# Kernel optimization log

Hardware: AMD Instinct MI355X
Metric: run time of the kernel (lower is better)

The kernel has to match this reference:

```python
import jax, jax.numpy as jnp
import numpy as np

N = 100000
IN_DIM = 128
HID = 128
HEADS = 2
OUT_DIM = 2
E = 800000
NEG_SLOPE = 0.2


def setup_inputs() -> dict:
    key = jax.random.key(0)
    ks = jax.random.split(key, 12)
    x = jax.random.normal(ks[0], (N, IN_DIM), dtype=jnp.float32)
    edge_index = jax.random.randint(ks[1], (2, E), 0, N, dtype=jnp.int64)
    s = 0.05
    # GATConv layer 1: in=128 -> heads=2, out=128
    W1 = jax.random.normal(ks[2], (IN_DIM, HEADS * HID), dtype=jnp.float32) * s
    a_src1 = jax.random.normal(ks[3], (HEADS, HID), dtype=jnp.float32) * s
    a_dst1 = jax.random.normal(ks[4], (HEADS, HID), dtype=jnp.float32) * s
    b1 = jnp.zeros((HEADS * HID,), dtype=jnp.float32)
    # GATConv layer 2: in=256 -> heads=2, out=128
    W2 = jax.random.normal(ks[5], (HEADS * HID, HEADS * HID), dtype=jnp.float32) * s
    a_src2 = jax.random.normal(ks[6], (HEADS, HID), dtype=jnp.float32) * s
    a_dst2 = jax.random.normal(ks[7], (HEADS, HID), dtype=jnp.float32) * s
    b2 = jnp.zeros((HEADS * HID,), dtype=jnp.float32)
    # post_mp: Linear(256,128) -> Dropout(eval, no-op) -> Linear(128,2)
    Wp1 = jax.random.normal(ks[8], (HEADS * HID, HID), dtype=jnp.float32) * s
    bp1 = jnp.zeros((HID,), dtype=jnp.float32)
    Wp2 = jax.random.normal(ks[9], (HID, OUT_DIM), dtype=jnp.float32) * s
    bp2 = jnp.zeros((OUT_DIM,), dtype=jnp.float32)
    return {"x": x, "edge_index": edge_index,
            "W1": W1, "a_src1": a_src1, "a_dst1": a_dst1, "b1": b1,
            "W2": W2, "a_src2": a_src2, "a_dst2": a_dst2, "b2": b2,
            "Wp1": Wp1, "bp1": bp1, "Wp2": Wp2, "bp2": bp2}


def gat_conv(x, src, dst, W, a_src, a_dst, b):
    # linear transform, split heads: [N, H, C]
    h = (x @ W).reshape(-1, HEADS, HID)
    # per-node attention logits: [N, H]
    alpha_src = jnp.sum(h * a_src, axis=-1)
    alpha_dst = jnp.sum(h * a_dst, axis=-1)
    # per-edge logits, edge e = (src -> dst): [E, H]
    e = jax.nn.leaky_relu(alpha_src[src] + alpha_dst[dst], NEG_SLOPE)
    # segment softmax over incoming edges of each destination node
    m = jax.ops.segment_max(e, dst, num_segments=N)
    e = jnp.exp(e - m[dst])
    denom = jax.ops.segment_sum(e, dst, num_segments=N)
    alpha = e / (denom[dst] + 1e-16)
    # gather source features, weight, scatter-add to destinations
    msg = h[src] * alpha[:, :, None]            # [E, H, C]
    out = jax.ops.segment_sum(msg, dst, num_segments=N)  # [N, H, C]
    return out.reshape(-1, HEADS * HID) + b


def reference(x, edge_index, W1, a_src1, a_dst1, b1, W2, a_src2, a_dst2, b2,
              Wp1, bp1, Wp2, bp2):
    # add self-loops (PyG GATConv default)
    loops = jnp.arange(N, dtype=edge_index.dtype)
    src = jnp.concatenate([edge_index[0], loops])
    dst = jnp.concatenate([edge_index[1], loops])
    h = jax.nn.relu(gat_conv(x, src, dst, W1, a_src1, a_dst1, b1))
    h = jax.nn.relu(gat_conv(h, src, dst, W2, a_src2, a_dst2, b2))
    h = h @ Wp1 + bp1          # post_mp Linear 1 (dropout is eval no-op)
    h = h @ Wp2 + bp2          # post_mp Linear 2
    return jax.nn.sigmoid(h)
```

## Files before the change

### kernel.cpp

```cpp
#include <hip/hip_runtime.h>
#include <hip/hip_bf16.h>
#include <math.h>

#define NNODES 100000
#define NPAD   100032
#define IN_DIM 128
#define HID 128
#define HEADS 2
#define F2 256
#define NEDGES 800000
#define ETOT 900000
#define NEG_SLOPE 0.2f

typedef unsigned int uint;
typedef unsigned short ushort;
typedef __attribute__((ext_vector_type(8))) short short8;
typedef __attribute__((ext_vector_type(4))) float floatx4;

__device__ __forceinline__ ushort f2bf(float f) {
    uint u = __builtin_bit_cast(uint, f);
    u += 0x7fffu + ((u >> 16) & 1u);
    return (ushort)(u >> 16);
}
__device__ __forceinline__ float bf2f(uint u16) {
    return __builtin_bit_cast(float, u16 << 16);
}
__device__ __forceinline__ float wred_sum(float v) {
    for (int o = 32; o; o >>= 1) v += __shfl_xor(v, o);
    return v;
}

__global__ __launch_bounds__(256) void hist_kernel(const int* __restrict__ ei,
                                                   int* __restrict__ deg) {
    int i = blockIdx.x * 256 + threadIdx.x;
    if (i >= ETOT) return;
    int dst = (i < NEDGES) ? ei[NEDGES + i] : (i - NEDGES);
    atomicAdd(&deg[dst], 1);
}

__global__ __launch_bounds__(256) void scan1_kernel(const int* __restrict__ deg,
                                                    int* __restrict__ row_start,
                                                    int* __restrict__ bsum) {
    __shared__ int s[256];
    int t = threadIdx.x;
    int i = blockIdx.x * 256 + t;
    int v = (i < NNODES) ? deg[i] : 0;
    s[t] = v;
    __syncthreads();
    for (int off = 1; off < 256; off <<= 1) {
        int x = (t >= off) ? s[t - off] : 0;
        __syncthreads();
        s[t] += x;
        __syncthreads();
    }
    if (i < NNODES) row_start[i] = s[t] - v;
    if (t == 255) bsum[blockIdx.x] = s[255];
}

__global__ __launch_bounds__(512) void scan2_kernel(const int* __restrict__ bsum,
                                                    int* __restrict__ bsum2,
                                                    int cnt) {
    __shared__ int s[512];
    int t = threadIdx.x;
    int v = (t < cnt) ? bsum[t] : 0;
    s[t] = v;
    __syncthreads();
    for (int off = 1; off < 512; off <<= 1) {
        int x = (t >= off) ? s[t - off] : 0;
        __syncthreads();
        s[t] += x;
        __syncthreads();
    }
    bsum2[t] = s[t] - v;
}

__global__ __launch_bounds__(256) void scan3_kernel(int* __restrict__ row_start,
                                                    const int* __restrict__ bsum2,
                                                    int* __restrict__ cursor) {
    int i = blockIdx.x * 256 + threadIdx.x;
    if (i == 0) row_start[NNODES] = ETOT;
    if (i >= NNODES) return;
    int r = row_start[i] + bsum2[i >> 8];
    row_start[i] = r;
    cursor[i] = r;
}

__global__ __launch_bounds__(256) void scatter_kernel(const int* __restrict__ ei,
                                                      int* __restrict__ cursor,
                                                      int* __restrict__ csr_src) {
    int i = blockIdx.x * 256 + threadIdx.x;
    if (i >= ETOT) return;
    int src, dst;
    if (i < NEDGES) { src = ei[i]; dst = ei[NEDGES + i]; }
    else            { src = i - NEDGES; dst = src; }
    int pos = atomicAdd(&cursor[dst], 1);
    csr_src[pos] = src;
}

__global__ __launch_bounds__(256) void transpose_bf_kernel(const float* __restrict__ W,
                                                           ushort* __restrict__ Wt,
                                                           int K, int N) {
    int i = blockIdx.x * 256 + threadIdx.x;
    if (i >= K * N) return;
    int n = i / K, k = i - n * K;
    Wt[(size_t)n * K + k] = f2bf(W[(size_t)k * N + n]);
}

__global__ __launch_bounds__(256) void fw_kernel(const float* __restrict__ Wp1,
                                                 const float* __restrict__ bp1,
                                                 const float* __restrict__ Wp2,
                                                 const float* __restrict__ bp2,
                                                 float2* __restrict__ Wf,
                                                 float* __restrict__ bfv) {
    int k = threadIdx.x;
    float s0 = 0.f, s1 = 0.f;
    for (int m = 0; m < 128; m++) {
        float w = Wp1[(size_t)k * 128 + m];
        s0 += w * Wp2[2 * m];
        s1 += w * Wp2[2 * m + 1];
    }
    Wf[k] = make_float2(s0, s1);
    if (k < 2) {
        float b = bp2[k];
        for (int m = 0; m < 128; m++) b += bp1[m] * Wp2[2 * m + k];
        bfv[k] = b;
    }
}

__global__ __launch_bounds__(256) void mfma_gemm_f32A(const float* __restrict__ A,
                                                      const ushort* __restrict__ Bt,
                                                      ushort* __restrict__ C,
                                                      float* __restrict__ as_f,
                                                      float* __restrict__ ad_f,
                                                      const float* __restrict__ aS,
                                                      const float* __restrict__ aD,
                                                      int K) {
    __shared__ ushort As[64][40];
    __shared__ ushort Bs[128][40];
    int t = threadIdx.x;
    int wave = t >> 6, lane = t & 63;
    int quad = lane >> 4, l16 = lane & 15;
    size_t rowBase = (size_t)blockIdx.x * 64;
    int colBase = blockIdx.y * 128;
    int head = blockIdx.y;

    floatx4 acc[8];
#pragma unroll
    for (int i = 0; i < 8; i++) acc[i] = (floatx4){0.f, 0.f, 0.f, 0.f};

    int ar = t >> 2, ac = (t & 3) * 8;
    int agr = (int)rowBase + ar;
    const float*  Ap  = A + (size_t)agr * K + ac;
    const ushort* Bp0 = Bt + (size_t)(colBase + ar) * K + ac;
    const ushort* Bp1 = Bp0 + (size_t)64 * K;
    bool aok = agr < NNODES;

    for (int k0 = 0; k0 < K; k0 += 32) {
        float4 f0 = make_float4(0.f, 0.f, 0.f, 0.f), f1 = f0;
        if (aok) {
            f0 = *reinterpret_cast<const float4*>(Ap + k0);
            f1 = *reinterpret_cast<const float4*>(Ap + k0 + 4);
        }
        uint4 b0 = *reinterpret_cast<const uint4*>(Bp0 + k0);
        uint4 b1 = *reinterpret_cast<const uint4*>(Bp1 + k0);
        uint4 av;
        av.x = (uint)f2bf(f0.x) | ((uint)f2bf(f0.y) << 16);
        av.y = (uint)f2bf(f0.z) | ((uint)f2bf(f0.w) << 16);
        av.z = (uint)f2bf(f1.x) | ((uint)f2bf(f1.y) << 16);
        av.w = (uint)f2bf(f1.z) | ((uint)f2bf(f1.w) << 16);
        *reinterpret_cast<uint4*>(&As[ar][ac])      = av;
        *reinterpret_cast<uint4*>(&Bs[ar][ac])      = b0;
        *reinterpret_cast<uint4*>(&Bs[64 + ar][ac]) = b1;
        __syncthreads();

        union { uint4 u; short8 s; } afr, bfr;
        afr.u = *reinterpret_cast<const uint4*>(&As[wave * 16 + l16][quad * 8]);
#pragma unroll
        for (int nt = 0; nt < 8; nt++) {
            bfr.u = *reinterpret_cast<const uint4*>(&Bs[nt * 16 + l16][quad * 8]);
            acc[nt] = __builtin_amdgcn_mfma_f32_16x16x32_bf16(afr.s, bfr.s, acc[nt], 0, 0, 0);
        }
        __syncthreads();
    }

#pragma unroll
    for (int nt = 0; nt < 8; nt++) {
        int col = colBase + nt * 16 + l16;
#pragma unroll
        for (int r = 0; r < 4; r++) {
            size_t row = rowBase + wave * 16 + quad * 4 + r;
            C[row * F2 + col] = f2bf(acc[nt][r]);
        }
    }
    float aSv[8], aDv[8];
#pragma unroll
    for (int nt = 0; nt < 8; nt++) {
        int c = colBase + nt * 16 + l16;
        aSv[nt] = aS[c];
        aDv[nt] = aD[c];
    }
#pragma unroll
    for (int r = 0; r < 4; r++) {
        float ps = 0.f, pd = 0.f;
#pragma unroll
        for (int nt = 0; nt < 8; nt++) {
            ps += acc[nt][r] * aSv[nt];
            pd += acc[nt][r] * aDv[nt];
        }
#pragma unroll
        for (int o = 1; o < 16; o <<= 1) {
            ps += __shfl_xor(ps, o);
            pd += __shfl_xor(pd, o);
        }
        if (l16 == 0) {
            size_t row = rowBase + wave * 16 + quad * 4 + r;
            as_f[2 * row + head] = ps;
            ad_f[2 * row + head] = pd;
        }
    }
}

__global__ __launch_bounds__(256) void mfma_gemm_bf16A(const ushort* __restrict__ A,
                                                       const ushort* __restrict__ Bt,
                                                       ushort* __restrict__ C,
                                                       float* __restrict__ as_f,
                                                       float* __restrict__ ad_f,
                                                       const float* __restrict__ aS,
                                                       const float* __restrict__ aD,
                                                       int K) {
    __shared__ ushort As[64][40];
    __shared__ ushort Bs[128][40];
    int t = threadIdx.x;
    int wave = t >> 6, lane = t & 63;
    int quad = lane >> 4, l16 = lane & 15;
    size_t rowBase = (size_t)blockIdx.x * 64;
    int colBase = blockIdx.y * 128;
    int head = blockIdx.y;

    floatx4 acc[8];
#pragma unroll
    for (int i = 0; i < 8; i++) acc[i] = (floatx4){0.f, 0.f, 0.f, 0.f};

    int ar = t >> 2, ac = (t & 3) * 8;
    const ushort* Ap  = A + (rowBase + ar) * K + ac;
    const ushort* Bp0 = Bt + (size_t)(colBase + ar) * K + ac;
    const ushort* Bp1 = Bp0 + (size_t)64 * K;

    for (int k0 = 0; k0 < K; k0 += 32) {
        uint4 av = *reinterpret_cast<const uint4*>(Ap + k0);
        uint4 b0 = *reinterpret_cast<const uint4*>(Bp0 + k0);
        uint4 b1 = *reinterpret_cast<const uint4*>(Bp1 + k0);
        *reinterpret_cast<uint4*>(&As[ar][ac])      = av;
        *reinterpret_cast<uint4*>(&Bs[ar][ac])      = b0;
        *reinterpret_cast<uint4*>(&Bs[64 + ar][ac]) = b1;
        __syncthreads();

        union { uint4 u; short8 s; } afr, bfr;
        afr.u = *reinterpret_cast<const uint4*>(&As[wave * 16 + l16][quad * 8]);
#pragma unroll
        for (int nt = 0; nt < 8; nt++) {
            bfr.u = *reinterpret_cast<const uint4*>(&Bs[nt * 16 + l16][quad * 8]);
            acc[nt] = __builtin_amdgcn_mfma_f32_16x16x32_bf16(afr.s, bfr.s, acc[nt], 0, 0, 0);
        }
        __syncthreads();
    }

#pragma unroll
    for (int nt = 0; nt < 8; nt++) {
        int col = colBase + nt * 16 + l16;
#pragma unroll
        for (int r = 0; r < 4; r++) {
            size_t row = rowBase + wave * 16 + quad * 4 + r;
            C[row * F2 + col] = f2bf(acc[nt][r]);
        }
    }
    float aSv[8], aDv[8];
#pragma unroll
    for (int nt = 0; nt < 8; nt++) {
        int c = colBase + nt * 16 + l16;
        aSv[nt] = aS[c];
        aDv[nt] = aD[c];
    }
#pragma unroll
    for (int r = 0; r < 4; r++) {
        float ps = 0.f, pd = 0.f;
#pragma unroll
        for (int nt = 0; nt < 8; nt++) {
            ps += acc[nt][r] * aSv[nt];
            pd += acc[nt][r] * aDv[nt];
        }
#pragma unroll
        for (int o = 1; o < 16; o <<= 1) {
            ps += __shfl_xor(ps, o);
            pd += __shfl_xor(pd, o);
        }
        if (l16 == 0) {
            size_t row = rowBase + wave * 16 + quad * 4 + r;
            as_f[2 * row + head] = ps;
            ad_f[2 * row + head] = pd;
        }
    }
}

__global__ __launch_bounds__(256) void gather_kernel(const uint2* __restrict__ hb2,
                                                     const int* __restrict__ row_start,
                                                     const int* __restrict__ csr_src,
                                                     const float2* __restrict__ as_,
                                                     const float2* __restrict__ ad_,
                                                     const float4* __restrict__ bias4,
                                                     uint2* __restrict__ outb2,
                                                     const float4* __restrict__ WfA,
                                                     const float* __restrict__ bfv,
                                                     float2* __restrict__ outp,
                                                     int final_mode) {
    int wave = threadIdx.x >> 6, lane = threadIdx.x & 63;
    int n = blockIdx.x * 4 + wave;
    if (n >= NNODES) return;
    int beg = row_start[n], end = row_start[n + 1];
    float2 ad = ad_[n];
    bool head1 = lane >= 32;

    float a0 = 0.f, a1 = 0.f, a2 = 0.f, a3 = 0.f;
    float aden = 0.f;

    for (int chunk = beg; chunk < end; chunk += 64) {
        int cnt = end - chunk;
        if (cnt > 64) cnt = 64;
        int e = chunk + lane;
        int sv = csr_src[(e < end) ? e : (end - 1)];
        float2 q = as_[sv];
        float l0 = q.x + ad.x; l0 = l0 > 0.f ? l0 : NEG_SLOPE * l0;
        float l1 = q.y + ad.y; l1 = l1 > 0.f ? l1 : NEG_SLOPE * l1;
        float w0 = __expf(l0);
        float w1 = __expf(l1);

#pragma unroll 4
        for (int j = 0; j < cnt; j++) {
            int   sj  = __builtin_amdgcn_readlane(sv, j);
            float wj0 = __builtin_bit_cast(float,
                          __builtin_amdgcn_readlane(__builtin_bit_cast(int, w0), j));
            float wj1 = __builtin_bit_cast(float,
                          __builtin_amdgcn_readlane(__builtin_bit_cast(int, w1), j));
            float wj = head1 ? wj1 : wj0;
            uint2 hv = hb2[(size_t)sj * 64 + lane];
            aden += wj;
            a0 += wj * bf2f(hv.x & 0xffffu);
            a1 += wj * bf2f(hv.x >> 16);
            a2 += wj * bf2f(hv.y & 0xffffu);
            a3 += wj * bf2f(hv.y >> 16);
        }
    }
    float inv = 1.f / (aden + 1e-16f);
    float4 b = bias4[lane];
    float o0 = fmaxf(a0 * inv + b.x, 0.f);
    float o1 = fmaxf(a1 * inv + b.y, 0.f);
    float o2 = fmaxf(a2 * inv + b.z, 0.f);
    float o3 = fmaxf(a3 * inv + b.w, 0.f);
    if (!final_mode) {
        uint2 pk;
        pk.x = (uint)f2bf(o0) | ((uint)f2bf(o1) << 16);
        pk.y = (uint)f2bf(o2) | ((uint)f2bf(o3) << 16);
        outb2[(size_t)n * 64 + lane] = pk;
    } else {
        float4 wa = WfA[2 * lane];
        float4 wb = WfA[2 * lane + 1];
        float p0 = o0 * wa.x + o1 * wa.z + o2 * wb.x + o3 * wb.z;
        float p1 = o0 * wa.y + o1 * wa.w + o2 * wb.y + o3 * wb.w;
        p0 = wred_sum(p0);
        p1 = wred_sum(p1);
        if (lane == 0) {
            float2 r;
            r.x = 1.f / (1.f + __expf(-(p0 + bfv[0])));
            r.y = 1.f / (1.f + __expf(-(p1 + bfv[1])));
            outp[n] = r;
        }
    }
}

extern "C" void kernel_launch(void* const* d_in, const int* in_sizes, int n_in,
                              void* d_out, int out_size, void* d_ws, size_t ws_size,
                              hipStream_t stream) {
    const float* x      = (const float*)d_in[0];
    const int*   ei     = (const int*)d_in[1];
    const float* W1     = (const float*)d_in[2];
    const float* a_src1 = (const float*)d_in[3];
    const float* a_dst1 = (const float*)d_in[4];
    const float* b1     = (const float*)d_in[5];
    const float* W2     = (const float*)d_in[6];
    const float* a_src2 = (const float*)d_in[7];
    const float* a_dst2 = (const float*)d_in[8];
    const float* b2     = (const float*)d_in[9];
    const float* Wp1    = (const float*)d_in[10];
    const float* bp1    = (const float*)d_in[11];
    const float* Wp2    = (const float*)d_in[12];
    const float* bp2    = (const float*)d_in[13];
    float* outp = (float*)d_out;

    char* w = (char*)d_ws;
    ushort* hbf  = (ushort*)w; w += (size_t)NPAD * 256 * sizeof(ushort);
    ushort* obf  = (ushort*)w; w += (size_t)NPAD * 256 * sizeof(ushort);
    ushort* W1t  = (ushort*)w; w += (size_t)256 * 128 * sizeof(ushort);
    ushort* W2t  = (ushort*)w; w += (size_t)256 * 256 * sizeof(ushort);
    float2* Wf   = (float2*)w; w += 256 * sizeof(float2);
    float*  bfv  = (float*)w;  w += 4 * sizeof(float);
    float2* as_  = (float2*)w; w += (size_t)NPAD * sizeof(float2);
    float2* ad_  = (float2*)w; w += (size_t)NPAD * sizeof(float2);
    int* deg       = (int*)w; w += (size_t)NNODES * sizeof(int);
    int* row_start = (int*)w; w += (size_t)(NNODES + 16) * sizeof(int);
    int* cursor    = (int*)w; w += (size_t)NNODES * sizeof(int);
    int* csr_src   = (int*)w; w += (size_t)ETOT * sizeof(int);
    int* bsum      = (int*)w; w += 512 * sizeof(int);
    int* bsum2     = (int*)w; w += 512 * sizeof(int);

    const int SCAN_BLOCKS = (NNODES + 255) / 256;
    const int NODE_WAVES  = (NNODES + 3) / 4;
    const int MB = NPAD / 64;

    hipMemsetAsync(deg, 0, (size_t)NNODES * sizeof(int), stream);
    hist_kernel<<<(ETOT + 255) / 256, 256, 0, stream>>>(ei, deg);
    scan1_kernel<<<SCAN_BLOCKS, 256, 0, stream>>>(deg, row_start, bsum);
    scan2_kernel<<<1, 512, 0, stream>>>(bsum, bsum2, SCAN_BLOCKS);
    scan3_kernel<<<SCAN_BLOCKS, 256, 0, stream>>>(row_start, bsum2, cursor);
    scatter_kernel<<<(ETOT + 255) / 256, 256, 0, stream>>>(ei, cursor, csr_src);

    transpose_bf_kernel<<<(128 * 256 + 255) / 256, 256, 0, stream>>>(W1, W1t, 128, 256);
    transpose_bf_kernel<<<(256 * 256 + 255) / 256, 256, 0, stream>>>(W2, W2t, 256, 256);
    fw_kernel<<<1, 256, 0, stream>>>(Wp1, bp1, Wp2, bp2, Wf, bfv);

    mfma_gemm_f32A<<<dim3(MB, 2), 256, 0, stream>>>(x, W1t, hbf, (float*)as_, (float*)ad_,
                                                    a_src1, a_dst1, 128);
    gather_kernel<<<NODE_WAVES, 256, 0, stream>>>((const uint2*)hbf, row_start, csr_src,
                                                  as_, ad_, (const float4*)b1, (uint2*)obf,
                                                  (const float4*)Wf, bfv, (float2*)outp, 0);

    mfma_gemm_bf16A<<<dim3(MB, 2), 256, 0, stream>>>(obf, W2t, hbf, (float*)as_, (float*)ad_,
                                                     a_src2, a_dst2, 256);
    gather_kernel<<<NODE_WAVES, 256, 0, stream>>>((const uint2*)hbf, row_start, csr_src,
                                                  as_, ad_, (const float4*)b2, (uint2*)obf,
                                                  (const float4*)Wf, bfv, (float2*)outp, 1);
}
```

Baseline: 448.7 us.

## Merge scan and weight-prep kernels; unroll gather loop by four edges

Merges scan2 and scan3 into one kernel where each block adds up the preceding block sums itself. Folds the two weight transposes and the post-MLP weight fold into a single prep kernel, cutting launch count. The gather kernel now processes four edges per iteration with direct loads and a per-lane exp, replacing the 64-edge chunk and readlane broadcast. This gives more independent loads in flight but repeats the exp and attention-logit loads on every lane.

```diff
diff --git a/kernel.cpp b/kernel.cpp
--- a/kernel.cpp
+++ b/kernel.cpp
@@ -57,32 +57,27 @@
     if (t == 255) bsum[blockIdx.x] = s[255];
 }
 
-__global__ __launch_bounds__(512) void scan2_kernel(const int* __restrict__ bsum,
-                                                    int* __restrict__ bsum2,
-                                                    int cnt) {
-    __shared__ int s[512];
-    int t = threadIdx.x;
-    int v = (t < cnt) ? bsum[t] : 0;
-    s[t] = v;
+__global__ __launch_bounds__(256) void scan_fix_kernel(int* __restrict__ row_start,
+                                                       const int* __restrict__ bsum,
+                                                       int* __restrict__ cursor) {
+    __shared__ int sh[256];
+    int t = threadIdx.x, bid = blockIdx.x;
+    int v = 0;
+    for (int k = t; k < bid; k += 256) v += bsum[k];
+    sh[t] = v;
     __syncthreads();
-    for (int off = 1; off < 512; off <<= 1) {
-        int x = (t >= off) ? s[t - off] : 0;
-        __syncthreads();
-        s[t] += x;
-        __syncthreads();
-    }
-    bsum2[t] = s[t] - v;
-}
-
-__global__ __launch_bounds__(256) void scan3_kernel(int* __restrict__ row_start,
-                                                    const int* __restrict__ bsum2,
-                                                    int* __restrict__ cursor) {
-    int i = blockIdx.x * 256 + threadIdx.x;
+    for (int off = 128; off; off >>= 1) {
+        if (t < off) sh[t] += sh[t + off];
+        __syncthreads();
+    }
+    int boff = sh[0];
+    int i = bid * 256 + t;
     if (i == 0) row_start[NNODES] = ETOT;
-    if (i >= NNODES) return;
-    int r = row_start[i] + bsum2[i >> 8];
-    row_start[i] = r;
-    cursor[i] = r;
+    if (i < NNODES) {
+        int r = row_start[i] + boff;
+        row_start[i] = r;
+        cursor[i] = r;
+    }
 }
 
 __global__ __launch_bounds__(256) void scatter_kernel(const int* __restrict__ ei,
@@ -97,33 +92,38 @@
     csr_src[pos] = src;
 }
 
-__global__ __launch_bounds__(256) void transpose_bf_kernel(const float* __restrict__ W,
-                                                           ushort* __restrict__ Wt,
-                                                           int K, int N) {
-    int i = blockIdx.x * 256 + threadIdx.x;
-    if (i >= K * N) return;
-    int n = i / K, k = i - n * K;
-    Wt[(size_t)n * K + k] = f2bf(W[(size_t)k * N + n]);
-}
-
-__global__ __launch_bounds__(256) void fw_kernel(const float* __restrict__ Wp1,
-                                                 const float* __restrict__ bp1,
-                                                 const float* __restrict__ Wp2,
-                                                 const float* __restrict__ bp2,
-                                                 float2* __restrict__ Wf,
-                                                 float* __restrict__ bfv) {
-    int k = threadIdx.x;
-    float s0 = 0.f, s1 = 0.f;
-    for (int m = 0; m < 128; m++) {
-        float w = Wp1[(size_t)k * 128 + m];
-        s0 += w * Wp2[2 * m];
-        s1 += w * Wp2[2 * m + 1];
-    }
-    Wf[k] = make_float2(s0, s1);
-    if (k < 2) {
-        float b = bp2[k];
-        for (int m = 0; m < 128; m++) b += bp1[m] * Wp2[2 * m + k];
-        bfv[k] = b;
+__global__ __launch_bounds__(256) void prep_kernel(const float* __restrict__ W1,
+                                                   ushort* __restrict__ W1t,
+                                                   const float* __restrict__ W2,
+                                                   ushort* __restrict__ W2t,
+                                                   const float* __restrict__ Wp1,
+                                                   const float* __restrict__ bp1,
+                                                   const float* __restrict__ Wp2,
+                                                   const float* __restrict__ bp2,
+                                                   float2* __restrict__ Wf,
+                                                   float* __restrict__ bfv) {
+    int b = blockIdx.x, t = threadIdx.x;
+    if (b < 128) {
+        int i = b * 256 + t;
+        int n = i >> 7, k = i & 127;
+        W1t[n * 128 + k] = f2bf(W1[k * 256 + n]);
+    } else if (b < 384) {
+        int i = (b - 128) * 256 + t;
+        int n = i >> 8, k = i & 255;
+        W2t[n * 256 + k] = f2bf(W2[k * 256 + n]);
+    } else {
+        float s0 = 0.f, s1 = 0.f;
+        for (int m = 0; m < 128; m++) {
+            float w = Wp1[t * 128 + m];
+            s0 += w * Wp2[2 * m];
+            s1 += w * Wp2[2 * m + 1];
+        }
+        Wf[t] = make_float2(s0, s1);
+        if (t < 2) {
+            float bb = bp2[t];
+            for (int m = 0; m < 128; m++) bb += bp1[m] * Wp2[2 * m + t];
+            bfv[t] = bb;
+        }
     }
 }
 
@@ -319,37 +319,66 @@
     int beg = row_start[n], end = row_start[n + 1];
     float2 ad = ad_[n];
     bool head1 = lane >= 32;
+    float adsel = head1 ? ad.y : ad.x;
 
     float a0 = 0.f, a1 = 0.f, a2 = 0.f, a3 = 0.f;
     float aden = 0.f;
-
-    for (int chunk = beg; chunk < end; chunk += 64) {
-        int cnt = end - chunk;
-        if (cnt > 64) cnt = 64;
-        int e = chunk + lane;
-        int sv = csr_src[(e < end) ? e : (end - 1)];
-        float2 q = as_[sv];
-        float l0 = q.x + ad.x; l0 = l0 > 0.f ? l0 : NEG_SLOPE * l0;
-        float l1 = q.y + ad.y; l1 = l1 > 0.f ? l1 : NEG_SLOPE * l1;
+    const char* hbase = (const char*)hb2;
+    uint laneoff = (uint)lane * 8u;
+
+    int j = beg;
+    for (; j + 3 < end; j += 4) {
+        int s0 = csr_src[j],     s1 = csr_src[j + 1];
+        int s2 = csr_src[j + 2], s3 = csr_src[j + 3];
+        float2 q0 = as_[s0], q1 = as_[s1], q2 = as_[s2], q3 = as_[s3];
+        uint2 h0 = *(const uint2*)(hbase + (size_t)(((uint)s0 << 9) + laneoff));
+        uint2 h1 = *(const uint2*)(hbase + (size_t)(((uint)s1 << 9) + laneoff));
+        uint2 h2 = *(const uint2*)(hbase + (size_t)(((uint)s2 << 9) + laneoff));
+        uint2 h3 = *(const uint2*)(hbase + (size_t)(((uint)s3 << 9) + laneoff));
+        float l0 = (head1 ? q0.y : q0.x) + adsel; l0 = l0 > 0.f ? l0 : NEG_SLOPE * l0;
+        float l1 = (head1 ? q1.y : q1.x) + adsel; l1 = l1 > 0.f ? l1 : NEG_SLOPE * l1;
+        float l2 = (head1 ? q2.y : q2.x) + adsel; l2 = l2 > 0.f ? l2 : NEG_SLOPE * l2;
+        float l3 = (head1 ? q3.y : q3.x) + adsel; l3 = l3 > 0.f ? l3 : NEG_SLOPE * l3;
+        float w0 = __expf(l0), w1 = __expf(l1), w2 = __expf(l2), w3 = __expf(l3);
+        aden += (w0 + w1) + (w2 + w3);
+        a0 += w0 * bf2f(h0.x & 0xffffu) + w1 * bf2f(h1.x & 0xffffu)
+            + w2 * bf2f(h2.x & 0xffffu) + w3 * bf2f(h3.x & 0xffffu);
+        a1 += w0 * bf2f(h0.x >> 16) + w1 * bf2f(h1.x >> 16)
+            + w2 * bf2f(h2.x >> 16) + w3 * bf2f(h3.x >> 16);
+        a2 += w0 * bf2f(h0.y & 0xffffu) + w1 * bf2f(h1.y & 0xffffu)
+            + w2 * bf2f(h2.y & 0xffffu) + w3 * bf2f(h3.y & 0xffffu);
+        a3 += w0 * bf2f(h0.y >> 16) + w1 * bf2f(h1.y >> 16)
+            + w2 * bf2f(h2.y >> 16) + w3 * bf2f(h3.y >> 16);
+    }
+    if (j < end) {
+        int e1 = j + 1 < end ? j + 1 : end - 1;
+        int e2 = j + 2 < end ? j + 2 : end - 1;
+        int e3 = j + 3 < end ? j + 3 : end - 1;
+        int s0 = csr_src[j], s1 = csr_src[e1], s2 = csr_src[e2], s3 = csr_src[e3];
+        float2 q0 = as_[s0], q1 = as_[s1], q2 = as_[s2], q3 = as_[s3];
+        uint2 h0 = *(const uint2*)(hbase + (size_t)(((uint)s0 << 9) + laneoff));
+        uint2 h1 = *(const uint2*)(hbase + (size_t)(((uint)s1 << 9) + laneoff));
+        uint2 h2 = *(const uint2*)(hbase + (size_t)(((uint)s2 << 9) + laneoff));
+        uint2 h3 = *(const uint2*)(hbase + (size_t)(((uint)s3 << 9) + laneoff));
+        float l0 = (head1 ? q0.y : q0.x) + adsel; l0 = l0 > 0.f ? l0 : NEG_SLOPE * l0;
+        float l1 = (head1 ? q1.y : q1.x) + adsel; l1 = l1 > 0.f ? l1 : NEG_SLOPE * l1;
+        float l2 = (head1 ? q2.y : q2.x) + adsel; l2 = l2 > 0.f ? l2 : NEG_SLOPE * l2;
+        float l3 = (head1 ? q3.y : q3.x) + adsel; l3 = l3 > 0.f ? l3 : NEG_SLOPE * l3;
         float w0 = __expf(l0);
-        float w1 = __expf(l1);
-
-#pragma unroll 4
-        for (int j = 0; j < cnt; j++) {
-            int   sj  = __builtin_amdgcn_readlane(sv, j);
-            float wj0 = __builtin_bit_cast(float,
-                          __builtin_amdgcn_readlane(__builtin_bit_cast(int, w0), j));
-            float wj1 = __builtin_bit_cast(float,
-                          __builtin_amdgcn_readlane(__builtin_bit_cast(int, w1), j));
-            float wj = head1 ? wj1 : wj0;
-            uint2 hv = hb2[(size_t)sj * 64 + lane];
-            aden += wj;
-            a0 += wj * bf2f(hv.x & 0xffffu);
-            a1 += wj * bf2f(hv.x >> 16);
-            a2 += wj * bf2f(hv.y & 0xffffu);
-            a3 += wj * bf2f(hv.y >> 16);
-        }
-    }
+        float w1 = (j + 1 < end) ? __expf(l1) : 0.f;
+        float w2 = (j + 2 < end) ? __expf(l2) : 0.f;
+        float w3 = (j + 3 < end) ? __expf(l3) : 0.f;
+        aden += (w0 + w1) + (w2 + w3);
+        a0 += w0 * bf2f(h0.x & 0xffffu) + w1 * bf2f(h1.x & 0xffffu)
+            + w2 * bf2f(h2.x & 0xffffu) + w3 * bf2f(h3.x & 0xffffu);
+        a1 += w0 * bf2f(h0.x >> 16) + w1 * bf2f(h1.x >> 16)
+            + w2 * bf2f(h2.x >> 16) + w3 * bf2f(h3.x >> 16);
+        a2 += w0 * bf2f(h0.y & 0xffffu) + w1 * bf2f(h1.y & 0xffffu)
+            + w2 * bf2f(h2.y & 0xffffu) + w3 * bf2f(h3.y & 0xffffu);
+        a3 += w0 * bf2f(h0.y >> 16) + w1 * bf2f(h1.y >> 16)
+            + w2 * bf2f(h2.y >> 16) + w3 * bf2f(h3.y >> 16);
+    }
+
     float inv = 1.f / (aden + 1e-16f);
     float4 b = bias4[lane];
     float o0 = fmaxf(a0 * inv + b.x, 0.f);
@@ -410,7 +439,6 @@
     int* cursor    = (int*)w; w += (size_t)NNODES * sizeof(int);
     int* csr_src   = (int*)w; w += (size_t)ETOT * sizeof(int);
     int* bsum      = (int*)w; w += 512 * sizeof(int);
-    int* bsum2     = (int*)w; w += 512 * sizeof(int);
 
     const int SCAN_BLOCKS = (NNODES + 255) / 256;
     const int NODE_WAVES  = (NNODES + 3) / 4;
@@ -419,13 +447,10 @@
     hipMemsetAsync(deg, 0, (size_t)NNODES * sizeof(int), stream);
     hist_kernel<<<(ETOT + 255) / 256, 256, 0, stream>>>(ei, deg);
     scan1_kernel<<<SCAN_BLOCKS, 256, 0, stream>>>(deg, row_start, bsum);
-    scan2_kernel<<<1, 512, 0, stream>>>(bsum, bsum2, SCAN_BLOCKS);
-    scan3_kernel<<<SCAN_BLOCKS, 256, 0, stream>>>(row_start, bsum2, cursor);
+    scan_fix_kernel<<<SCAN_BLOCKS, 256, 0, stream>>>(row_start, bsum, cursor);
     scatter_kernel<<<(ETOT + 255) / 256, 256, 0, stream>>>(ei, cursor, csr_src);
 
-    transpose_bf_kernel<<<(128 * 256 + 255) / 256, 256, 0, stream>>>(W1, W1t, 128, 256);
-    transpose_bf_kernel<<<(256 * 256 + 255) / 256, 256, 0, stream>>>(W2, W2t, 256, 256);
-    fw_kernel<<<1, 256, 0, stream>>>(Wp1, bp1, Wp2, bp2, Wf, bfv);
+    prep_kernel<<<385, 256, 0, stream>>>(W1, W1t, W2, W2t, Wp1, bp1, Wp2, bp2, Wf, bfv);
 
     mfma_gemm_f32A<<<dim3(MB, 2), 256, 0, stream>>>(x, W1t, hbf, (float*)as_, (float*)ad_,
                                                     a_src1, a_dst1, 128);
```

Measured after the change: 436.6 us. 2.7% less time.
